# Performance work log

Hardware: AMD Instinct MI355X
Metric: run time of the kernel (lower is better)

The kernel has to match this reference:

```python
import jax, jax.numpy as jnp
import numpy as np

ATTENTION_HEAD = 16
EXPANSION_LENGTH = 300
TEXT_EMBEDDING_DIM = 768
LN_EPS = 1e-3  # keras LayerNormalization default epsilon


def setup_inputs() -> dict:
    key = jax.random.key(0)
    ks = jax.random.split(key, 8)
    B, L, D = 8, 2048, TEXT_EMBEDDING_DIM
    H = ATTENTION_HEAD
    E = EXPANSION_LENGTH
    dh = D // H
    glorot = lambda k, shape, fan_in, fan_out: jax.random.uniform(
        k, shape, jnp.float32,
        -jnp.sqrt(6.0 / (fan_in + fan_out)), jnp.sqrt(6.0 / (fan_in + fan_out)))
    return {
        "q": jax.random.normal(ks[0], (B, 1, L, D), jnp.float32),
        "k": jax.random.normal(ks[1], (B, 1, L, D), jnp.float32),
        "v": jax.random.normal(ks[2], (B, 1, L, D), jnp.float32),
        "Wq": glorot(ks[3], (D, D), D, D),
        "bq": jnp.zeros((D,), jnp.float32),
        "Wv": glorot(ks[4], (D, D), D, D),
        "bv": jnp.zeros((D,), jnp.float32),
        "memory": glorot(ks[5], (E, H, dh), E, dh),
        "gamma": jnp.ones((D,), jnp.float32),
        "beta": jnp.zeros((D,), jnp.float32),
    }


def reference(q, k, v, Wq, bq, Wv, bv, memory, gamma, beta):
    B, _, L, D = q.shape
    H = ATTENTION_HEAD
    dh = D // H
    # Dense projections (v is unused by the original module)
    Q_ = q @ Wq + bq                      # (B,1,L,D)
    V_ = k @ Wv + bv                      # (B,1,L,D)
    Q = Q_.reshape(B, L, H, dh)
    V = V_.reshape(B, L, H, dh)
    # memory-query scores, ReLU instead of softmax
    eij = jax.nn.relu(jnp.einsum('ehd,blhd->belh', memory, Q))  # (B,E,L,H)
    out1 = jnp.einsum('belh,blhd->behd', eij, V)                # (B,E,H,dh)
    out2 = jnp.einsum('behd,belh->blhd', out1, eij)             # (B,L,H,dh)
    x = out2.reshape(B, 1, L, D)
    mean = jnp.mean(x, axis=-1, keepdims=True)
    var = jnp.var(x, axis=-1, keepdims=True)
    return (x - mean) * jax.lax.rsqrt(var + LN_EPS) * gamma + beta
```

## Files before the change

kernel.cpp:

```cpp
#include <hip/hip_runtime.h>
#include <hip/hip_bf16.h>
#include <stdint.h>

#define B_   8
#define L_   2048
#define D_   768
#define H_   16
#define DH   48
#define E_   300
#define EP   320
#define KP   64
#define ACH  8
#define N1T  (128 * DH * EP)
#define NT_  24

typedef __bf16 bf16;
typedef __bf16 bf16x8 __attribute__((ext_vector_type(8)));
typedef __bf16 bf16x4 __attribute__((ext_vector_type(4)));
typedef float  f32x4  __attribute__((ext_vector_type(4)));

typedef const __attribute__((address_space(1))) uint32_t guint;
typedef __attribute__((address_space(3))) uint32_t luint;

__device__ __forceinline__ f32x4 mfma16(bf16x8 a, bf16x8 b, f32x4 c) {
  return __builtin_amdgcn_mfma_f32_16x16x32_bf16(a, b, c, 0, 0, 0);
}

__global__ __launch_bounds__(256) void k_cast(const float* __restrict__ q,
                                              const float* __restrict__ k,
                                              bf16* __restrict__ qc,
                                              bf16* __restrict__ kc) {
  const float* src = blockIdx.y ? k : q;
  bf16* dst = blockIdx.y ? kc : qc;
  const int n8 = B_ * L_ * D_ / 8;
  for (int i = blockIdx.x * 256 + threadIdx.x; i < n8; i += gridDim.x * 256) {
    float4 f0 = *(const float4*)(src + (size_t)i * 8);
    float4 f1 = *(const float4*)(src + (size_t)i * 8 + 4);
    bf16x8 v;
    v[0] = (bf16)f0.x; v[1] = (bf16)f0.y; v[2] = (bf16)f0.z; v[3] = (bf16)f0.w;
    v[4] = (bf16)f1.x; v[5] = (bf16)f1.y; v[6] = (bf16)f1.z; v[7] = (bf16)f1.w;
    *(bf16x8*)(dst + (size_t)i * 8) = v;
  }
}

__global__ __launch_bounds__(256) void k_wt(const float* __restrict__ Wq,
                                            const float* __restrict__ Wv,
                                            bf16* __restrict__ WqT,
                                            bf16* __restrict__ WvT) {
  int idx = blockIdx.x * 256 + threadIdx.x;
  int n = idx / D_, k = idx % D_;
  const float* W = blockIdx.y ? Wv : Wq;
  bf16* WT = blockIdx.y ? WvT : WqT;
  WT[n * D_ + k] = (bf16)W[k * D_ + n];
}

__global__ __launch_bounds__(256) void k_mem(const float* __restrict__ M,
                                             bf16* __restrict__ MP) {
  int idx = blockIdx.x * 256 + threadIdx.x;
  int h = idx / (EP * KP);
  int r = idx % (EP * KP);
  int e = r / KP, d = r % KP;
  float v = (e < E_ && d < DH) ? M[(e * H_ + h) * DH + d] : 0.f;
  MP[idx] = (bf16)v;
}

__global__ __launch_bounds__(256, 3) void k_gemm(
    const bf16* __restrict__ A0, const bf16* __restrict__ A1,
    const bf16* __restrict__ WT0, const bf16* __restrict__ WT1,
    const float* __restrict__ b0, const float* __restrict__ b1,
    bf16* __restrict__ outQ, bf16* __restrict__ outVT) {
  __shared__ bf16 As[3][128 * 32];
  __shared__ bf16 Bs[3][128 * 32];
  const int tid = threadIdx.x, lane = tid & 63, w = tid >> 6;
  const int wr = w >> 1, wc = w & 1;
  const int lr = lane & 15, lq = lane >> 4;
  const int bid = blockIdx.x;
  const int j = (bid & 7) * 96 + (bid >> 3);
  const int n0 = (j % 6) * 128, m0 = (j / 6) * 128;
  const int mode = blockIdx.y;
  const bf16* A = mode ? A1 : A0;
  const bf16* WT = mode ? WT1 : WT0;
  const float* bias = mode ? b1 : b0;

  auto stage = [&](int buf, int k0) {
#pragma unroll
    for (int p = 0; p < 2; ++p) {
      int idx = tid + p * 256;
      int row = idx >> 2, ct = idx & 3;
      int gc = ct ^ ((row >> 1) & 3);
      const bf16* src = A + (size_t)(m0 + row) * D_ + k0 + gc * 8;
      __builtin_amdgcn_global_load_lds((guint*)src,
          (luint*)&As[buf][(p * 256 + w * 64) * 8], 16, 0, 0);
    }
#pragma unroll
    for (int p = 0; p < 2; ++p) {
      int idx = tid + p * 256;
      int row = idx >> 2, ct = idx & 3;
      int gc = ct ^ ((row >> 1) & 3);
      const bf16* src = WT + (size_t)(n0 + row) * D_ + k0 + gc * 8;
      __builtin_amdgcn_global_load_lds((guint*)src,
          (luint*)&Bs[buf][(p * 256 + w * 64) * 8], 16, 0, 0);
    }
  };

  f32x4 acc[4][4] = {};

  stage(0, 0);
  stage(1, 32);

  for (int t = 0; t < NT_; ++t) {
    const int cur = t % 3;
    if (t + 1 < NT_) asm volatile("s_waitcnt vmcnt(4) lgkmcnt(0)" ::: "memory");
    else             asm volatile("s_waitcnt vmcnt(0) lgkmcnt(0)" ::: "memory");
    __builtin_amdgcn_s_barrier();
    __builtin_amdgcn_sched_barrier(0);
    if (t + 2 < NT_) stage((t + 2) % 3, (t + 2) * 32);

    bf16x8 af[4], bfr[4];
#pragma unroll
    for (int mi = 0; mi < 4; ++mi) {
      int row = wr * 64 + mi * 16 + lr;
      af[mi] = *(const bf16x8*)&As[cur][row * 32 + ((lq ^ ((row >> 1) & 3)) * 8)];
    }
#pragma unroll
    for (int ni = 0; ni < 4; ++ni) {
      int row = wc * 64 + ni * 16 + lr;
      bfr[ni] = *(const bf16x8*)&Bs[cur][row * 32 + ((lq ^ ((row >> 1) & 3)) * 8)];
    }
#pragma unroll
    for (int mi = 0; mi < 4; ++mi)
#pragma unroll
      for (int ni = 0; ni < 4; ++ni)
        acc[mi][ni] = mfma16(af[mi], bfr[ni], acc[mi][ni]);
  }

  float bs[4];
#pragma unroll
  for (int ni = 0; ni < 4; ++ni) bs[ni] = bias[n0 + wc * 64 + ni * 16 + lr];

  if (mode == 0) {
#pragma unroll
    for (int mi = 0; mi < 4; ++mi)
#pragma unroll
      for (int ni = 0; ni < 4; ++ni) {
        int m = m0 + wr * 64 + mi * 16 + lq * 4;
        int n = n0 + wc * 64 + ni * 16 + lr;
#pragma unroll
        for (int r = 0; r < 4; ++r)
          outQ[(size_t)(m + r) * D_ + n] = (bf16)(acc[mi][ni][r] + bs[ni]);
      }
  } else {
#pragma unroll
    for (int mi = 0; mi < 4; ++mi)
#pragma unroll
      for (int ni = 0; ni < 4; ++ni) {
        int mb = m0 + wr * 64 + mi * 16 + lq * 4;
        int n = n0 + wc * 64 + ni * 16 + lr;
        int bhd = (mb >> 11) * H_ + n / DH;
        int d = n % DH;
        int l = mb & (L_ - 1);
        bf16x4 v;
#pragma unroll
        for (int r = 0; r < 4; ++r) v[r] = (bf16)(acc[mi][ni][r] + bs[ni]);
        *(bf16x4*)&outVT[((size_t)bhd * DH + d) * L_ + l] = v;
      }
  }
}

__global__ __launch_bounds__(256) void k_phaseA(
    const bf16* __restrict__ Qb, const bf16* __restrict__ VT,
    const bf16* __restrict__ MP, bf16* __restrict__ O1P) {
  __shared__ bf16 Qs[2][32 * 88];
  __shared__ bf16 Vs[2][48 * 40];
  __shared__ bf16 Ss[EP * 40];
  const int tid = threadIdx.x, lane = tid & 63, w = tid >> 6;
  const int lr = lane & 15, lq = lane >> 4;
  const int bh = blockIdx.y, b = bh >> 4, h = bh & 15;
  const int lbase = blockIdx.x * (L_ / ACH);

  bf16x8 mf[5][2];
#pragma unroll
  for (int mi = 0; mi < 5; ++mi)
#pragma unroll
    for (int kh = 0; kh < 2; ++kh)
      mf[mi][kh] = *(const bf16x8*)&MP[(size_t)(h * EP + w * 80 + mi * 16 + lr) * KP + kh * 32 + lq * 8];

  if (tid < 128) {
    int buf = tid >> 6, t = tid & 63;
    uint4 z = {0, 0, 0, 0};
    *(uint4*)&Qs[buf][(t >> 1) * 88 + 48 + (t & 1) * 8] = z;
  }

  auto loadQ = [&](int idx, int l0) {
    return *(const bf16x8*)&Qb[(size_t)(b * L_ + l0 + idx / 6) * D_ + h * DH + (idx % 6) * 8];
  };
  auto loadV = [&](int j, int l0) {
    return *(const bf16x8*)&VT[((size_t)bh * DH + (j >> 2)) * L_ + l0 + (j & 3) * 8];
  };

  bf16x8 rA, rB;
  {
    int l0 = lbase;
    rA = (tid < 192) ? loadQ(tid, l0) : loadV(tid - 192, l0);
    if (tid < 128) rB = loadV(tid + 64, l0);
  }

  f32x4 acc[5][3] = {};

  for (int it = 0; it < L_ / ACH / 32; ++it) {
    const int cur = it & 1;
    if (tid < 192) *(bf16x8*)&Qs[cur][(tid / 6) * 88 + (tid % 6) * 8] = rA;
    else           *(bf16x8*)&Vs[cur][((tid - 192) >> 2) * 40 + ((tid - 192) & 3) * 8] = rA;
    if (tid < 128) *(bf16x8*)&Vs[cur][((tid + 64) >> 2) * 40 + ((tid + 64) & 3) * 8] = rB;
    __syncthreads();
    if (it + 1 < L_ / ACH / 32) {
      int l0 = lbase + (it + 1) * 32;
      rA = (tid < 192) ? loadQ(tid, l0) : loadV(tid - 192, l0);
      if (tid < 128) rB = loadV(tid + 64, l0);
    }
    bf16x8 qf[2][2];
#pragma unroll
    for (int ni = 0; ni < 2; ++ni)
#pragma unroll
      for (int kh = 0; kh < 2; ++kh)
        qf[ni][kh] = *(const bf16x8*)&Qs[cur][(ni * 16 + lr) * 88 + kh * 32 + lq * 8];
#pragma unroll
    for (int mi = 0; mi < 5; ++mi)
#pragma unroll
      for (int ni = 0; ni < 2; ++ni) {
        f32x4 s = {0.f, 0.f, 0.f, 0.f};
        s = mfma16(mf[mi][0], qf[ni][0], s);
        s = mfma16(mf[mi][1], qf[ni][1], s);
#pragma unroll
        for (int r = 0; r < 4; ++r)
          Ss[(w * 80 + mi * 16 + lq * 4 + r) * 40 + ni * 16 + lr] =
              (bf16)(s[r] > 0.f ? s[r] : 0.f);
      }
    bf16x8 sf[5], vf[3];
#pragma unroll
    for (int mi = 0; mi < 5; ++mi)
      sf[mi] = *(const bf16x8*)&Ss[(w * 80 + mi * 16 + lr) * 40 + lq * 8];
#pragma unroll
    for (int ni = 0; ni < 3; ++ni)
      vf[ni] = *(const bf16x8*)&Vs[cur][(ni * 16 + lr) * 40 + lq * 8];
#pragma unroll
    for (int mi = 0; mi < 5; ++mi)
#pragma unroll
      for (int ni = 0; ni < 3; ++ni)
        acc[mi][ni] = mfma16(sf[mi], vf[ni], acc[mi][ni]);
  }
  bf16* dst = O1P + (size_t)(blockIdx.x * 128 + bh) * DH * EP;
#pragma unroll
  for (int mi = 0; mi < 5; ++mi)
#pragma unroll
    for (int ni = 0; ni < 3; ++ni) {
      int e = w * 80 + mi * 16 + lq * 4;
      int d = ni * 16 + lr;
      bf16x4 v;
#pragma unroll
      for (int r = 0; r < 4; ++r) v[r] = (bf16)acc[mi][ni][r];
      *(bf16x4*)&dst[(size_t)d * EP + e] = v;
    }
}

__global__ __launch_bounds__(256) void k_red(const bf16* __restrict__ O1P,
                                             bf16* __restrict__ O1T) {
  int i8 = blockIdx.x * 256 + threadIdx.x;
  if (i8 >= N1T / 8) return;
  float s[8] = {};
#pragma unroll
  for (int c = 0; c < ACH; ++c) {
    bf16x8 v = *(const bf16x8*)&O1P[(size_t)c * N1T + (size_t)i8 * 8];
#pragma unroll
    for (int j = 0; j < 8; ++j) s[j] += (float)v[j];
  }
  bf16x8 o;
#pragma unroll
  for (int j = 0; j < 8; ++j) o[j] = (bf16)s[j];
  *(bf16x8*)&O1T[(size_t)i8 * 8] = o;
}

__global__ __launch_bounds__(256, 4) void k_phaseB(
    const bf16* __restrict__ Qb, const bf16* __restrict__ MP,
    const bf16* __restrict__ O1T, bf16* __restrict__ X) {
  __shared__ bf16 Qs[64 * 88];
  __shared__ bf16 STs[64 * 76];
  __shared__ bf16 O1s[2][48 * 76];
  const int tid = threadIdx.x, lane = tid & 63, w = tid >> 6;
  const int lr = lane & 15, lq = lane >> 4;
  const int bh = blockIdx.y, b = bh >> 4, h = bh & 15;
  const int l0 = blockIdx.x * 64;

  bf16x8 mfB[5][2];
#pragma unroll
  for (int c = 0; c < 5; ++c)
#pragma unroll
    for (int kh = 0; kh < 2; ++kh)
      mfB[c][kh] = *(const bf16x8*)&MP[(size_t)(h * EP + c * 64 + w * 16 + lr) * KP + kh * 32 + lq * 8];

  for (int idx = tid; idx < 512; idx += 256) {
    if (idx < 384) {
      int row = idx / 6, c = idx % 6;
      *(bf16x8*)&Qs[row * 88 + c * 8] =
          *(const bf16x8*)&Qb[(size_t)(b * L_ + l0 + row) * D_ + h * DH + c * 8];
    } else {
      int j = idx - 384;
      uint4 z = {0, 0, 0, 0};
      *(uint4*)&Qs[(j >> 1) * 88 + 48 + (j & 1) * 8] = z;
    }
  }
  for (int idx = tid; idx < 384; idx += 256)
    *(bf16x8*)&O1s[0][(idx >> 3) * 76 + (idx & 7) * 8] =
        *(const bf16x8*)&O1T[((size_t)bh * DH + (idx >> 3)) * EP + (idx & 7) * 8];
  __syncthreads();

  f32x4 acc[3] = {};
#pragma unroll
  for (int c = 0; c < 5; ++c) {
    bf16x8 r0, r1;
    if (c < 4) {
      r0 = *(const bf16x8*)&O1T[((size_t)bh * DH + (tid >> 3)) * EP + (c + 1) * 64 + (tid & 7) * 8];
      if (tid < 128) {
        int i2 = tid + 256;
        r1 = *(const bf16x8*)&O1T[((size_t)bh * DH + (i2 >> 3)) * EP + (c + 1) * 64 + (i2 & 7) * 8];
      }
    }
#pragma unroll
    for (int mi = 0; mi < 4; ++mi) {
      bf16x8 qa0 = *(const bf16x8*)&Qs[(mi * 16 + lr) * 88 + lq * 8];
      bf16x8 qa1 = *(const bf16x8*)&Qs[(mi * 16 + lr) * 88 + 32 + lq * 8];
      f32x4 s = {0.f, 0.f, 0.f, 0.f};
      s = mfma16(qa0, mfB[c][0], s);
      s = mfma16(qa1, mfB[c][1], s);
#pragma unroll
      for (int r = 0; r < 4; ++r)
        STs[(mi * 16 + lq * 4 + r) * 76 + w * 16 + lr] =
            (bf16)(s[r] > 0.f ? s[r] : 0.f);
    }
    __syncthreads();
#pragma unroll
    for (int ks = 0; ks < 2; ++ks) {
      bf16x8 sf = *(const bf16x8*)&STs[(w * 16 + lr) * 76 + ks * 32 + lq * 8];
#pragma unroll
      for (int ni = 0; ni < 3; ++ni) {
        bf16x8 of = *(const bf16x8*)&O1s[c & 1][(ni * 16 + lr) * 76 + ks * 32 + lq * 8];
        acc[ni] = mfma16(sf, of, acc[ni]);
      }
    }
    if (c < 4) {
      *(bf16x8*)&O1s[(c + 1) & 1][(tid >> 3) * 76 + (tid & 7) * 8] = r0;
      if (tid < 128) {
        int i2 = tid + 256;
        *(bf16x8*)&O1s[(c + 1) & 1][(i2 >> 3) * 76 + (i2 & 7) * 8] = r1;
      }
    }
    __syncthreads();
  }
#pragma unroll
  for (int ni = 0; ni < 3; ++ni)
#pragma unroll
    for (int r = 0; r < 4; ++r)
      X[(size_t)(b * L_ + l0 + w * 16 + lq * 4 + r) * D_ + h * DH + ni * 16 + lr] =
          (bf16)acc[ni][r];
}

__global__ __launch_bounds__(256) void k_ln(
    const bf16* __restrict__ X, const float* __restrict__ gamma,
    const float* __restrict__ beta, float* __restrict__ out) {
  const int lane = threadIdx.x & 63;
  const int row = blockIdx.x * 4 + (threadIdx.x >> 6);
  const bf16* x = X + (size_t)row * D_;
  float v[12];
#pragma unroll
  for (int c = 0; c < 3; ++c) {
    bf16x4 ch = *(const bf16x4*)(x + lane * 12 + c * 4);
#pragma unroll
    for (int j = 0; j < 4; ++j) v[c * 4 + j] = (float)ch[j];
  }
  float s = 0.f, q = 0.f;
#pragma unroll
  for (int j = 0; j < 12; ++j) { s += v[j]; q += v[j] * v[j]; }
#pragma unroll
  for (int off = 32; off > 0; off >>= 1) {
    s += __shfl_xor(s, off);
    q += __shfl_xor(q, off);
  }
  float mean = s * (1.f / 768.f);
  float var = q * (1.f / 768.f) - mean * mean;
  float inv = rsqrtf(var + 1e-3f);
  float* o = out + (size_t)row * D_;
#pragma unroll
  for (int c = 0; c < 3; ++c) {
    float4 g = *(const float4*)(gamma + lane * 12 + c * 4);
    float4 bt = *(const float4*)(beta + lane * 12 + c * 4);
    float4 r;
    r.x = (v[c * 4 + 0] - mean) * inv * g.x + bt.x;
    r.y = (v[c * 4 + 1] - mean) * inv * g.y + bt.y;
    r.z = (v[c * 4 + 2] - mean) * inv * g.z + bt.z;
    r.w = (v[c * 4 + 3] - mean) * inv * g.w + bt.w;
    *(float4*)(o + lane * 12 + c * 4) = r;
  }
}

extern "C" void kernel_launch(void* const* d_in, const int* in_sizes, int n_in,
                              void* d_out, int out_size, void* d_ws, size_t ws_size,
                              hipStream_t stream) {
  (void)in_sizes; (void)n_in; (void)out_size; (void)ws_size;
  const float* q_in = (const float*)d_in[0];
  const float* k_in = (const float*)d_in[1];
  const float* Wq   = (const float*)d_in[3];
  const float* bq   = (const float*)d_in[4];
  const float* Wv   = (const float*)d_in[5];
  const float* bv   = (const float*)d_in[6];
  const float* mem  = (const float*)d_in[7];
  const float* gam  = (const float*)d_in[8];
  const float* bet  = (const float*)d_in[9];
  float* out = (float*)d_out;

  char* ws = (char*)d_ws;
  size_t off = 0;
  auto alloc = [&](size_t bytes) {
    char* p = ws + off;
    off += (bytes + 255) & ~(size_t)255;
    return p;
  };
  bf16*  WqT = (bf16*)alloc((size_t)D_ * D_ * 2);
  bf16*  WvT = (bf16*)alloc((size_t)D_ * D_ * 2);
  bf16*  MP  = (bf16*)alloc((size_t)H_ * EP * KP * 2);
  bf16*  Qb  = (bf16*)alloc((size_t)B_ * L_ * D_ * 2);
  bf16*  VT  = (bf16*)alloc((size_t)B_ * H_ * DH * L_ * 2);
  bf16*  O1T = (bf16*)alloc((size_t)N1T * 2);
  const size_t castHalf  = ((size_t)B_ * L_ * D_ * 2 + 256) & ~(size_t)255;
  const size_t castBytes = 2 * castHalf;
  const size_t o1pBytes  = (size_t)ACH * N1T * 2;
  size_t bigBytes = castBytes > o1pBytes ? castBytes : o1pBytes;
  char*  big = alloc(bigBytes);
  bf16*  qc  = (bf16*)big;
  bf16*  kc  = (bf16*)(big + castHalf);
  bf16*  O1P = (bf16*)big;
  bf16*  Xb  = (bf16*)big;

  k_cast<<<dim3(2048, 2), 256, 0, stream>>>(q_in, k_in, qc, kc);
  k_wt<<<dim3((D_ * D_) / 256, 2), 256, 0, stream>>>(Wq, Wv, WqT, WvT);
  k_mem<<<(H_ * EP * KP) / 256, 256, 0, stream>>>(mem, MP);
  k_gemm<<<dim3(768, 2), 256, 0, stream>>>(qc, kc, WqT, WvT, bq, bv, Qb, VT);
  k_phaseA<<<dim3(ACH, B_ * H_), 256, 0, stream>>>(Qb, VT, MP, O1P);
  k_red<<<(N1T / 8 + 255) / 256, 256, 0, stream>>>(O1P, O1T);
  k_phaseB<<<dim3(L_ / 64, B_ * H_), 256, 0, stream>>>(Qb, MP, O1T, Xb);
  k_ln<<<(B_ * L_) / 4, 256, 0, stream>>>(Xb, gam, bet, out);
}
```

Before: 190.7 us.

## Merge prep kernels, add MFMA priority hints, remap blocks across XCDs, unroll GEMM loop

Merges the weight-transpose and memory-padding kernels into one launch to save a kernel launch. Wraps the MFMA sections in the GEMM, phaseA and phaseB kernels with s_setprio raises so waves issuing matrix ops get scheduling priority. Remaps the 1D block index in phaseA and phaseB so consecutive blocks spread over the 8 XCDs while blocks sharing data stay together for L2 locality. Fully unrolls the GEMM k-loop, which may raise register pressure and code size.

```diff
diff --git a/kernel.cpp b/kernel.cpp
--- a/kernel.cpp
+++ b/kernel.cpp
@@ -43,25 +43,26 @@
   }
 }
 
-__global__ __launch_bounds__(256) void k_wt(const float* __restrict__ Wq,
-                                            const float* __restrict__ Wv,
-                                            bf16* __restrict__ WqT,
-                                            bf16* __restrict__ WvT) {
-  int idx = blockIdx.x * 256 + threadIdx.x;
-  int n = idx / D_, k = idx % D_;
-  const float* W = blockIdx.y ? Wv : Wq;
-  bf16* WT = blockIdx.y ? WvT : WqT;
-  WT[n * D_ + k] = (bf16)W[k * D_ + n];
-}
-
-__global__ __launch_bounds__(256) void k_mem(const float* __restrict__ M,
-                                             bf16* __restrict__ MP) {
-  int idx = blockIdx.x * 256 + threadIdx.x;
-  int h = idx / (EP * KP);
-  int r = idx % (EP * KP);
-  int e = r / KP, d = r % KP;
-  float v = (e < E_ && d < DH) ? M[(e * H_ + h) * DH + d] : 0.f;
-  MP[idx] = (bf16)v;
+__global__ __launch_bounds__(256) void k_prep(
+    const float* __restrict__ Wq, const float* __restrict__ Wv,
+    const float* __restrict__ M, bf16* __restrict__ WqT,
+    bf16* __restrict__ WvT, bf16* __restrict__ MP) {
+  int bid = blockIdx.x;
+  if (bid < 4608) {
+    int which = bid / 2304;
+    int idx = (bid % 2304) * 256 + threadIdx.x;
+    int n = idx / D_, k = idx % D_;
+    const float* W = which ? Wv : Wq;
+    bf16* WT = which ? WvT : WqT;
+    WT[n * D_ + k] = (bf16)W[k * D_ + n];
+  } else {
+    int idx = (bid - 4608) * 256 + threadIdx.x;
+    int h = idx / (EP * KP);
+    int r = idx % (EP * KP);
+    int e = r / KP, d = r % KP;
+    float v = (e < E_ && d < DH) ? M[(e * H_ + h) * DH + d] : 0.f;
+    MP[idx] = (bf16)v;
+  }
 }
 
 __global__ __launch_bounds__(256, 3) void k_gemm(
@@ -108,6 +109,7 @@
   stage(0, 0);
   stage(1, 32);
 
+#pragma unroll
   for (int t = 0; t < NT_; ++t) {
     const int cur = t % 3;
     if (t + 1 < NT_) asm volatile("s_waitcnt vmcnt(4) lgkmcnt(0)" ::: "memory");
@@ -127,11 +129,13 @@
       int row = wc * 64 + ni * 16 + lr;
       bfr[ni] = *(const bf16x8*)&Bs[cur][row * 32 + ((lq ^ ((row >> 1) & 3)) * 8)];
     }
+    __builtin_amdgcn_s_setprio(1);
 #pragma unroll
     for (int mi = 0; mi < 4; ++mi)
 #pragma unroll
       for (int ni = 0; ni < 4; ++ni)
         acc[mi][ni] = mfma16(af[mi], bfr[ni], acc[mi][ni]);
+    __builtin_amdgcn_s_setprio(0);
   }
 
   float bs[4];
@@ -175,8 +179,11 @@
   __shared__ bf16 Ss[EP * 40];
   const int tid = threadIdx.x, lane = tid & 63, w = tid >> 6;
   const int lr = lane & 15, lq = lane >> 4;
-  const int bh = blockIdx.y, b = bh >> 4, h = bh & 15;
-  const int lbase = blockIdx.x * (L_ / ACH);
+  const int bid = blockIdx.x;
+  const int jj = (bid & 7) * 128 + (bid >> 3);
+  const int bh = jj >> 3, b = bh >> 4, h = bh & 15;
+  const int ach = jj & 7;
+  const int lbase = ach * (L_ / ACH);
 
   bf16x8 mf[5][2];
 #pragma unroll
@@ -224,6 +231,7 @@
 #pragma unroll
       for (int kh = 0; kh < 2; ++kh)
         qf[ni][kh] = *(const bf16x8*)&Qs[cur][(ni * 16 + lr) * 88 + kh * 32 + lq * 8];
+    __builtin_amdgcn_s_setprio(1);
 #pragma unroll
     for (int mi = 0; mi < 5; ++mi)
 #pragma unroll
@@ -236,6 +244,7 @@
           Ss[(w * 80 + mi * 16 + lq * 4 + r) * 40 + ni * 16 + lr] =
               (bf16)(s[r] > 0.f ? s[r] : 0.f);
       }
+    __builtin_amdgcn_s_setprio(0);
     bf16x8 sf[5], vf[3];
 #pragma unroll
     for (int mi = 0; mi < 5; ++mi)
@@ -243,13 +252,15 @@
 #pragma unroll
     for (int ni = 0; ni < 3; ++ni)
       vf[ni] = *(const bf16x8*)&Vs[cur][(ni * 16 + lr) * 40 + lq * 8];
+    __builtin_amdgcn_s_setprio(1);
 #pragma unroll
     for (int mi = 0; mi < 5; ++mi)
 #pragma unroll
       for (int ni = 0; ni < 3; ++ni)
         acc[mi][ni] = mfma16(sf[mi], vf[ni], acc[mi][ni]);
-  }
-  bf16* dst = O1P + (size_t)(blockIdx.x * 128 + bh) * DH * EP;
+    __builtin_amdgcn_s_setprio(0);
+  }
+  bf16* dst = O1P + (size_t)(ach * 128 + bh) * DH * EP;
 #pragma unroll
   for (int mi = 0; mi < 5; ++mi)
 #pragma unroll
@@ -288,8 +299,10 @@
   __shared__ bf16 O1s[2][48 * 76];
   const int tid = threadIdx.x, lane = tid & 63, w = tid >> 6;
   const int lr = lane & 15, lq = lane >> 4;
-  const int bh = blockIdx.y, b = bh >> 4, h = bh & 15;
-  const int l0 = blockIdx.x * 64;
+  const int bid = blockIdx.x;
+  const int jj = (bid & 7) * 512 + (bid >> 3);
+  const int bh = jj >> 5, b = bh >> 4, h = bh & 15;
+  const int l0 = (jj & 31) * 64;
 
   bf16x8 mfB[5][2];
 #pragma unroll
@@ -325,6 +338,7 @@
         r1 = *(const bf16x8*)&O1T[((size_t)bh * DH + (i2 >> 3)) * EP + (c + 1) * 64 + (i2 & 7) * 8];
       }
     }
+    __builtin_amdgcn_s_setprio(1);
 #pragma unroll
     for (int mi = 0; mi < 4; ++mi) {
       bf16x8 qa0 = *(const bf16x8*)&Qs[(mi * 16 + lr) * 88 + lq * 8];
@@ -337,7 +351,9 @@
         STs[(mi * 16 + lq * 4 + r) * 76 + w * 16 + lr] =
             (bf16)(s[r] > 0.f ? s[r] : 0.f);
     }
+    __builtin_amdgcn_s_setprio(0);
     __syncthreads();
+    __builtin_amdgcn_s_setprio(1);
 #pragma unroll
     for (int ks = 0; ks < 2; ++ks) {
       bf16x8 sf = *(const bf16x8*)&STs[(w * 16 + lr) * 76 + ks * 32 + lq * 8];
@@ -347,6 +363,7 @@
         acc[ni] = mfma16(sf, of, acc[ni]);
       }
     }
+    __builtin_amdgcn_s_setprio(0);
     if (c < 4) {
       *(bf16x8*)&O1s[(c + 1) & 1][(tid >> 3) * 76 + (tid & 7) * 8] = r0;
       if (tid < 128) {
@@ -441,11 +458,10 @@
   bf16*  Xb  = (bf16*)big;
 
   k_cast<<<dim3(2048, 2), 256, 0, stream>>>(q_in, k_in, qc, kc);
-  k_wt<<<dim3((D_ * D_) / 256, 2), 256, 0, stream>>>(Wq, Wv, WqT, WvT);
-  k_mem<<<(H_ * EP * KP) / 256, 256, 0, stream>>>(mem, MP);
+  k_prep<<<5888, 256, 0, stream>>>(Wq, Wv, mem, WqT, WvT, MP);
   k_gemm<<<dim3(768, 2), 256, 0, stream>>>(qc, kc, WqT, WvT, bq, bv, Qb, VT);
-  k_phaseA<<<dim3(ACH, B_ * H_), 256, 0, stream>>>(Qb, VT, MP, O1P);
+  k_phaseA<<<1024, 256, 0, stream>>>(Qb, VT, MP, O1P);
   k_red<<<(N1T / 8 + 255) / 256, 256, 0, stream>>>(O1P, O1T);
-  k_phaseB<<<dim3(L_ / 64, B_ * H_), 256, 0, stream>>>(Qb, MP, O1T, Xb);
+  k_phaseB<<<4096, 256, 0, stream>>>(Qb, MP, O1T, Xb);
   k_ln<<<(B_ * L_) / 4, 256, 0, stream>>>(Xb, gam, bet, out);
 }
```

Result: no change. 191.9 us (+0.7%).
